# Performance work log

Hardware: AMD Instinct MI355X
Metric: run time of the kernel (lower is better)

The kernel has to match this reference:

```python
import jax, jax.numpy as jnp
import numpy as np

D_MODEL = 512
NUM_HEADS = 8
DEPTH = D_MODEL // NUM_HEADS


def setup_inputs() -> dict:
    key = jax.random.key(0)
    kx, kq, kk, kv, ko = jax.random.split(key, 5)
    scale = 1.0 / np.sqrt(D_MODEL)
    return {
        "x": jax.random.normal(kx, (4, 2048, D_MODEL), dtype=jnp.float32),
        "W_q": jax.random.normal(kq, (D_MODEL, D_MODEL), dtype=jnp.float32) * scale,
        "W_k": jax.random.normal(kk, (D_MODEL, D_MODEL), dtype=jnp.float32) * scale,
        "W_v": jax.random.normal(kv, (D_MODEL, D_MODEL), dtype=jnp.float32) * scale,
        "W_o": jax.random.normal(ko, (D_MODEL, D_MODEL), dtype=jnp.float32) * scale,
    }


def reference(x, W_q, W_k, W_v, W_o):
    B, S, _ = x.shape
    # nn.Linear with weight W: y = x @ W.T
    def split_heads(t):
        return t.reshape(B, S, NUM_HEADS, DEPTH).transpose(0, 2, 1, 3)  # [B,H,S,D]
    Q = split_heads(x @ W_q.T)
    K = split_heads(x @ W_k.T)
    V = split_heads(x @ W_v.T)
    b = -jnp.log(jnp.asarray(S, dtype=jnp.float32))  # -log(seq_len) bias
    inv_sqrt_dk = 1.0 / jnp.sqrt(jnp.asarray(DEPTH, dtype=jnp.float32))
    qk = jnp.einsum('bhqd,bhkd->bhqk', Q, K) * inv_sqrt_dk
    attn = jax.nn.sigmoid(qk + b)  # non-softmax sigmoid attention
    out = jnp.einsum('bhqk,bhkd->bhqd', attn, V)
    out = out.transpose(0, 2, 1, 3).reshape(B, S, D_MODEL)
    return out @ W_o.T
```

## Files before the change

kernel.cpp:

```cpp
#include <hip/hip_runtime.h>
#include <stdint.h>

typedef _Float16 f16x8 __attribute__((ext_vector_type(8)));
typedef _Float16 f16x4 __attribute__((ext_vector_type(4)));
typedef __fp16 h16x2 __attribute__((ext_vector_type(2)));
typedef float f32x4 __attribute__((ext_vector_type(4)));
typedef float f32x16 __attribute__((ext_vector_type(16)));

#define SEQ 2048
#define NHEADS 8

#define GLOAD_LDS16(gp, lp)                                                        \
  __builtin_amdgcn_global_load_lds(                                                \
      (const __attribute__((address_space(1))) void*)(uintptr_t)(const void*)(gp), \
      (__attribute__((address_space(3))) void*)(uintptr_t)(void*)(lp), 16, 0, 0)

#define GLD16(dst, ptr, imm) \
  asm volatile("global_load_dwordx4 %0, %1, off offset:%c2" : "=&v"(dst) : "v"(ptr), "i"(imm))

#define VMW(n)                                                     \
  do {                                                             \
    asm volatile("s_waitcnt vmcnt(%c0)" ::"i"(n) : "memory");      \
    __builtin_amdgcn_sched_barrier(0);                             \
  } while (0)

__device__ __forceinline__ f16x4 pack4(float a, float b, float c, float d) {
  h16x2 lo = __builtin_amdgcn_cvt_pkrtz(a, b);
  h16x2 hi = __builtin_amdgcn_cvt_pkrtz(c, d);
  f16x4 o;
  o.x = (_Float16)lo.x; o.y = (_Float16)lo.y;
  o.z = (_Float16)hi.x; o.w = (_Float16)hi.y;
  return o;
}

__global__ void cvt_all_kernel(const float* __restrict__ x, const float* __restrict__ wq,
                               const float* __restrict__ wk, const float* __restrict__ wv,
                               const float* __restrict__ wo, _Float16* __restrict__ xh,
                               _Float16* __restrict__ wh) {
  int i = blockIdx.x * 256 + threadIdx.x;
  const float* src;
  _Float16* dst;
  int off;
  if (i < 1048576) {
    src = x; dst = xh; off = i;
  } else {
    int j = i - 1048576;
    int sel = j >> 16;
    off = j & 65535;
    src = (sel == 0) ? wq : (sel == 1) ? wk : (sel == 2) ? wv : wo;
    dst = wh + (size_t)sel * 262144;
  }
  float4 v = ((const float4*)src)[off];
  ((f16x4*)dst)[off] = pack4(v.x, v.y, v.z, v.w);
}

__device__ __forceinline__ void gemm_tile_bt(const _Float16* __restrict__ A,
                                             const _Float16* __restrict__ B,
                                             int m0, int n0,
                                             _Float16* lds,
                                             f32x4 (&acc)[4][4]) {
  const int tid = threadIdx.x;
  const int w = tid >> 6, lane = tid & 63;
  const int wr = w >> 1, wc = w & 1;
  const int lrow = lane & 15, q = lane >> 4;
  const int snb = w * 32 + (lane >> 3);
  const int scb = lane & 7;

#pragma unroll
  for (int i = 0; i < 4; ++i)
#pragma unroll
    for (int j = 0; j < 4; ++j)
#pragma unroll
      for (int r = 0; r < 4; ++r) acc[i][j][r] = 0.f;

#pragma unroll
  for (int t = 0; t < 4; ++t) {
    int n = snb + t * 8;
    int cbg = scb ^ (n & 7);
    GLOAD_LDS16(A + (size_t)(m0 + n) * 512 + cbg * 8, lds + (w * 32 + t * 8) * 64);
    GLOAD_LDS16(B + (size_t)(n0 + n) * 512 + cbg * 8, lds + 8192 + (w * 32 + t * 8) * 64);
  }

  for (int kt = 0; kt < 8; ++kt) {
    __syncthreads();
    if (kt < 7) {
      _Float16* nb = lds + ((kt + 1) & 1) * 16384;
#pragma unroll
      for (int t = 0; t < 4; ++t) {
        int n = snb + t * 8;
        int cbg = scb ^ (n & 7);
        GLOAD_LDS16(A + (size_t)(m0 + n) * 512 + (kt + 1) * 64 + cbg * 8, nb + (w * 32 + t * 8) * 64);
        GLOAD_LDS16(B + (size_t)(n0 + n) * 512 + (kt + 1) * 64 + cbg * 8, nb + 8192 + (w * 32 + t * 8) * 64);
      }
    }
    _Float16* As = lds + (kt & 1) * 16384;
    _Float16* Bs = As + 8192;

    f16x8 af[4][2], bfr[4][2];
#pragma unroll
    for (int i = 0; i < 4; ++i) {
      int m = wr * 64 + i * 16 + lrow;
#pragma unroll
      for (int kk = 0; kk < 2; ++kk) {
        int cb = (kk * 4 + q) ^ (m & 7);
        af[i][kk] = *(const f16x8*)(As + m * 64 + cb * 8);
      }
    }
#pragma unroll
    for (int j = 0; j < 4; ++j) {
      int n = wc * 64 + j * 16 + lrow;
#pragma unroll
      for (int kk = 0; kk < 2; ++kk) {
        int cb = (kk * 4 + q) ^ (n & 7);
        bfr[j][kk] = *(const f16x8*)(Bs + n * 64 + cb * 8);
      }
    }
#pragma unroll
    for (int i = 0; i < 4; ++i)
#pragma unroll
      for (int j = 0; j < 4; ++j) {
        acc[i][j] = __builtin_amdgcn_mfma_f32_16x16x32_f16(af[i][0], bfr[j][0], acc[i][j], 0, 0, 0);
        acc[i][j] = __builtin_amdgcn_mfma_f32_16x16x32_f16(af[i][1], bfr[j][1], acc[i][j], 0, 0, 0);
      }
  }
}

__global__ __launch_bounds__(256, 2) void qkv_kernel(
    const _Float16* __restrict__ xb, const _Float16* __restrict__ Wq,
    const _Float16* __restrict__ Wk, const _Float16* __restrict__ Wv,
    _Float16* __restrict__ Qo, _Float16* __restrict__ Ko, _Float16* __restrict__ Vto) {
  __shared__ _Float16 pool[32768];
  const int z = blockIdx.z;
  f32x4 acc[4][4];
  const int tid = threadIdx.x, w = tid >> 6, lane = tid & 63;
  const int wr = w >> 1, wc = w & 1, lcol = lane & 15, q = lane >> 4;

  if (z < 2) {
    const int m0 = blockIdx.y * 128;
    const int n0 = blockIdx.x * 128;
    gemm_tile_bt((z == 0) ? Wq : Wk, xb, m0, n0, pool, acc);
    _Float16* outp = (z == 0) ? Qo : Ko;
    __syncthreads();
#pragma unroll
    for (int i = 0; i < 4; ++i) {
      int cl = wr * 64 + i * 16 + q * 4;
      int hh_l = cl >> 6, dd = cl & 63;
      int s4 = dd >> 4, hi2 = (dd >> 3) & 1, j0 = dd & 7;
#pragma unroll
      for (int j = 0; j < 4; ++j) {
        int s = wc * 64 + j * 16 + lcol;
        int blk = s >> 5, r32 = s & 31;
        int l32 = (z == 0) ? r32
                           : ((r32 & 3) | ((r32 & 4) << 1) | ((r32 & 8) >> 1) | (r32 & 16));
        *(f16x4*)(pool + (hh_l * 4 + blk) * 2048 + s4 * 512 + ((hi2 << 5) | l32) * 8 + j0) =
            pack4(acc[i][j][0], acc[i][j][1], acc[i][j][2], acc[i][j][3]);
      }
    }
    __syncthreads();
    {
      int b2 = n0 >> 11, sblk0 = (n0 & 2047) >> 5, hh0 = m0 >> 6;
#pragma unroll
      for (int rec = 0; rec < 8; ++rec) {
        int hh_l = rec >> 2, blk = rec & 3;
        size_t goff = (size_t)(b2 * NHEADS + hh0 + hh_l) * 131072 +
                      (size_t)(sblk0 + blk) * 2048;
        f16x8 vv = *(const f16x8*)(pool + rec * 2048 + tid * 8);
        *(f16x8*)(outp + goff + tid * 8) = vv;
      }
    }
  } else {
    const int m0 = blockIdx.x * 128;
    const int n0 = blockIdx.y * 128;
    gemm_tile_bt(xb, Wv, m0, n0, pool, acc);
    const int bb = m0 >> 11;
    __syncthreads();
#pragma unroll
    for (int i = 0; i < 4; ++i) {
      int s0 = wr * 64 + i * 16 + q * 4;
      int mi_l = s0 >> 5, kk = (s0 >> 4) & 1, hi2 = (s0 >> 3) & 1, j0 = s0 & 7;
#pragma unroll
      for (int j = 0; j < 4; ++j) {
        int c = wc * 64 + j * 16 + lcol;
        int hh_l = c >> 6, dd = c & 63;
        int t = dd >> 5, qq = dd & 31;
        *(f16x4*)(pool + (hh_l * 4 + mi_l) * 2048 + (kk * 2 + t) * 512 + ((hi2 << 5) | qq) * 8 + j0) =
            pack4(acc[i][j][0], acc[i][j][1], acc[i][j][2], acc[i][j][3]);
      }
    }
    __syncthreads();
    {
      int kblk0 = (m0 & 2047) >> 5, hh0 = n0 >> 6;
#pragma unroll
      for (int rec = 0; rec < 8; ++rec) {
        int hh_l = rec >> 2, mi_l = rec & 3;
        size_t goff = (size_t)(bb * NHEADS + hh0 + hh_l) * 131072 +
                      (size_t)(kblk0 + mi_l) * 2048;
        f16x8 vv = *(const f16x8*)(pool + rec * 2048 + tid * 8);
        *(f16x8*)(Vto + goff + tid * 8) = vv;
      }
    }
  }
}

__device__ __forceinline__ void attn_window(const f16x8 (&ka)[4], const f16x8 (&vb)[4],
                                            const f16x8 (&qb)[4], const f32x16& z16,
                                            f32x16& o0, f32x16& o1) {
  const float c1 = 0.18033688011112042f;
  __builtin_amdgcn_s_setprio(1);
  f32x16 s = __builtin_amdgcn_mfma_f32_32x32x16_f16(ka[0], qb[0], z16, 0, 0, 0);
  s = __builtin_amdgcn_mfma_f32_32x32x16_f16(ka[1], qb[1], s, 0, 0, 0);
  s = __builtin_amdgcn_mfma_f32_32x32x16_f16(ka[2], qb[2], s, 0, 0, 0);
  s = __builtin_amdgcn_mfma_f32_32x32x16_f16(ka[3], qb[3], s, 0, 0, 0);
  __builtin_amdgcn_s_setprio(0);

  float p[16];
#pragma unroll
  for (int r = 0; r < 16; ++r) {
    float wp = __builtin_amdgcn_exp2f(__builtin_fmaf(s[r], c1, -1.0f));
    float e = wp * 0.0009765625f;
    p[r] = __builtin_fmaf(wp, __builtin_fmaf(e, e, -e), wp);
  }

  f16x8 pa0, pa1;
  {
    h16x2 a0 = __builtin_amdgcn_cvt_pkrtz(p[0], p[1]);
    h16x2 a1 = __builtin_amdgcn_cvt_pkrtz(p[2], p[3]);
    h16x2 a2 = __builtin_amdgcn_cvt_pkrtz(p[4], p[5]);
    h16x2 a3 = __builtin_amdgcn_cvt_pkrtz(p[6], p[7]);
    pa0[0] = (_Float16)a0.x; pa0[1] = (_Float16)a0.y;
    pa0[2] = (_Float16)a1.x; pa0[3] = (_Float16)a1.y;
    pa0[4] = (_Float16)a2.x; pa0[5] = (_Float16)a2.y;
    pa0[6] = (_Float16)a3.x; pa0[7] = (_Float16)a3.y;
    h16x2 b0 = __builtin_amdgcn_cvt_pkrtz(p[8], p[9]);
    h16x2 b1 = __builtin_amdgcn_cvt_pkrtz(p[10], p[11]);
    h16x2 b2 = __builtin_amdgcn_cvt_pkrtz(p[12], p[13]);
    h16x2 b3 = __builtin_amdgcn_cvt_pkrtz(p[14], p[15]);
    pa1[0] = (_Float16)b0.x; pa1[1] = (_Float16)b0.y;
    pa1[2] = (_Float16)b1.x; pa1[3] = (_Float16)b1.y;
    pa1[4] = (_Float16)b2.x; pa1[5] = (_Float16)b2.y;
    pa1[6] = (_Float16)b3.x; pa1[7] = (_Float16)b3.y;
  }

  __builtin_amdgcn_s_setprio(1);
  o0 = __builtin_amdgcn_mfma_f32_32x32x16_f16(pa0, vb[0], o0, 0, 0, 0);
  o1 = __builtin_amdgcn_mfma_f32_32x32x16_f16(pa0, vb[1], o1, 0, 0, 0);
  o0 = __builtin_amdgcn_mfma_f32_32x32x16_f16(pa1, vb[2], o0, 0, 0, 0);
  o1 = __builtin_amdgcn_mfma_f32_32x32x16_f16(pa1, vb[3], o1, 0, 0, 0);
  __builtin_amdgcn_s_setprio(0);
}

#define ISSUE_WIN(KA, VB, KP, VP)  \
  do {                             \
    GLD16(KA[0], KP, 0);           \
    GLD16(KA[1], KP, 1024);        \
    GLD16(KA[2], KP, 2048);        \
    GLD16(KA[3], KP, 3072);        \
    GLD16(VB[0], VP, 0);           \
    GLD16(VB[1], VP, 1024);        \
    GLD16(VB[2], VP, 2048);        \
    GLD16(VB[3], VP, 3072);        \
    KP += 8192;                    \
    VP += 8192;                    \
  } while (0)

__global__ __launch_bounds__(256, 3) void attn_kernel(
    const _Float16* __restrict__ QF, const _Float16* __restrict__ KF,
    const _Float16* __restrict__ VF, _Float16* __restrict__ Ow) {
  __shared__ float Of[8704];

  const int tid = threadIdx.x, wv = tid >> 6, lane = tid & 63;
  const int q31 = lane & 31, hi = lane >> 5;

  const int L = blockIdx.x;
  const int xcd = L & 7, slot = L >> 3;
  const int bh = xcd * 4 + (slot >> 5), qt = slot & 31;
  const int b = bh >> 3, h = bh & 7;
  const int q0 = qt * 64;

  const int qi = wv & 1;
  const int kh = wv >> 1;
  const int qc = qt * 2 + qi;

  const char* qp = (const char*)QF + (size_t)bh * 262144 + qc * 4096 + lane * 16;
  const char* kpA = (const char*)KF + (size_t)bh * 262144 + (size_t)kh * 131072 + lane * 16;
  const char* kpB = kpA + 4096;
  const char* vpA = (const char*)VF + (size_t)bh * 262144 + (size_t)kh * 131072 + lane * 16;
  const char* vpB = vpA + 4096;

  f16x8 qb[4];
  GLD16(qb[0], qp, 0);
  GLD16(qb[1], qp, 1024);
  GLD16(qb[2], qp, 2048);
  GLD16(qb[3], qp, 3072);

  f16x8 kaA[4], vbA[4], kaB[4], vbB[4];
  ISSUE_WIN(kaA, vbA, kpA, vpA);
  ISSUE_WIN(kaB, vbB, kpB, vpB);

  f32x16 oacc0, oacc1, z16;
#pragma unroll
  for (int r = 0; r < 16; ++r) { z16[r] = 0.f; oacc0[r] = 0.f; oacc1[r] = 0.f; }

  for (int i = 0; i < 15; ++i) {
    VMW(8);
    attn_window(kaA, vbA, qb, z16, oacc0, oacc1);
    ISSUE_WIN(kaA, vbA, kpA, vpA);
    VMW(8);
    attn_window(kaB, vbB, qb, z16, oacc0, oacc1);
    ISSUE_WIN(kaB, vbB, kpB, vpB);
  }
  VMW(8);
  attn_window(kaA, vbA, qb, z16, oacc0, oacc1);
  VMW(0);
  attn_window(kaB, vbB, qb, z16, oacc0, oacc1);

#pragma unroll
  for (int t = 0; t < 2; ++t) {
#pragma unroll
    for (int r = 0; r < 16; ++r) {
      int row = qi * 32 + (r & 3) + ((r >> 2) << 3) + hi * 4;
      int d = t * 32 + q31;
      float v = (t == 0) ? oacc0[r] : oacc1[r];
      Of[kh * 4352 + row * 68 + d] = v * 0.0009765625f;
    }
  }
  __syncthreads();
#pragma unroll
  for (int i = 0; i < 4; ++i) {
    int o = tid * 16 + i * 4;
    int row = o >> 6, d0 = o & 63;
    f32x4 a = *(const f32x4*)(Of + row * 68 + d0);
    f32x4 c = *(const f32x4*)(Of + 4352 + row * 68 + d0);
    f16x4 v;
    v[0] = (_Float16)(a[0] + c[0]);
    v[1] = (_Float16)(a[1] + c[1]);
    v[2] = (_Float16)(a[2] + c[2]);
    v[3] = (_Float16)(a[3] + c[3]);
    *(f16x4*)(Ow + (size_t)(b * SEQ + q0 + row) * 512 + h * 64 + d0) = v;
  }
}

__global__ __launch_bounds__(256, 2) void oproj_kernel(
    const _Float16* __restrict__ A, const _Float16* __restrict__ Wo,
    float* __restrict__ out) {
  __shared__ _Float16 pool[32768];
  const int m0 = blockIdx.x * 128, n0 = blockIdx.y * 128;
  f32x4 acc[4][4];
  gemm_tile_bt(A, Wo, m0, n0, pool, acc);

  const int tid = threadIdx.x, w = tid >> 6, lane = tid & 63;
  const int wr = w >> 1, wc = w & 1, lcol = lane & 15, q = lane >> 4;
#pragma unroll
  for (int i = 0; i < 4; ++i) {
    int gm0 = m0 + wr * 64 + i * 16 + q * 4;
#pragma unroll
    for (int j = 0; j < 4; ++j) {
      int gn = n0 + wc * 64 + j * 16 + lcol;
#pragma unroll
      for (int r = 0; r < 4; ++r)
        out[(size_t)(gm0 + r) * 512 + gn] = acc[i][j][r];
    }
  }
}

extern "C" void kernel_launch(void* const* d_in, const int* in_sizes, int n_in,
                              void* d_out, int out_size, void* d_ws, size_t ws_size,
                              hipStream_t stream) {
  const float* x = (const float*)d_in[0];
  const float* Wq = (const float*)d_in[1];
  const float* Wk = (const float*)d_in[2];
  const float* Wv = (const float*)d_in[3];
  const float* Wo = (const float*)d_in[4];
  float* out = (float*)d_out;
  char* ws = (char*)d_ws;

  _Float16* xh = (_Float16*)(ws + 0);
  _Float16* wh = (_Float16*)(ws + 8388608);
  _Float16* Qw = (_Float16*)(ws + 10485760);
  _Float16* Kw = (_Float16*)(ws + 18874368);
  _Float16* Vtw = (_Float16*)(ws + 27262976);
  _Float16* Ow = (_Float16*)(ws + 35651584);

  _Float16* wqh = wh;
  _Float16* wkh = wh + 262144;
  _Float16* wvh = wh + 524288;
  _Float16* woh = wh + 786432;

  cvt_all_kernel<<<5120, 256, 0, stream>>>(x, Wq, Wk, Wv, Wo, xh, wh);
  qkv_kernel<<<dim3(64, 4, 3), 256, 0, stream>>>(xh, wqh, wkh, wvh, Qw, Kw, Vtw);
  attn_kernel<<<1024, 256, 0, stream>>>(Qw, Kw, Vtw, Ow);
  oproj_kernel<<<dim3(64, 4), 256, 0, stream>>>(Ow, woh, out);
}
```

Before: 152.6 us.

## Stage K/V windows through LDS via direct global-to-LDS loads, raise occupancy

Replaces the double-buffered register K/V prefetch with per-wave LDS staging using global_load_lds, read back with ds_read_b128 each iteration. Cutting register pressure lets launch_bounds go from 3 to 4 blocks per CU. The sigmoid polynomial is also packed into f32x2 vector FMAs. The single-buffered LDS stage forces a full vmcnt(0) wait every iteration, so load latency is only hidden by the extra occupancy rather than by in-wave prefetch.

```diff
diff --git a/kernel.cpp b/kernel.cpp
--- a/kernel.cpp
+++ b/kernel.cpp
@@ -4,6 +4,7 @@
 typedef _Float16 f16x8 __attribute__((ext_vector_type(8)));
 typedef _Float16 f16x4 __attribute__((ext_vector_type(4)));
 typedef __fp16 h16x2 __attribute__((ext_vector_type(2)));
+typedef float f32x2 __attribute__((ext_vector_type(2)));
 typedef float f32x4 __attribute__((ext_vector_type(4)));
 typedef float f32x16 __attribute__((ext_vector_type(16)));
 
@@ -18,9 +19,18 @@
 #define GLD16(dst, ptr, imm) \
   asm volatile("global_load_dwordx4 %0, %1, off offset:%c2" : "=&v"(dst) : "v"(ptr), "i"(imm))
 
+#define DSR(dst, base, imm) \
+  asm volatile("ds_read_b128 %0, %1 offset:%c2" : "=&v"(dst) : "v"(base), "i"(imm))
+
 #define VMW(n)                                                     \
   do {                                                             \
     asm volatile("s_waitcnt vmcnt(%c0)" ::"i"(n) : "memory");      \
+    __builtin_amdgcn_sched_barrier(0);                             \
+  } while (0)
+
+#define LGKM0()                                                    \
+  do {                                                             \
+    asm volatile("s_waitcnt lgkmcnt(0)" ::: "memory");             \
     __builtin_amdgcn_sched_barrier(0);                             \
   } while (0)
 
@@ -205,7 +215,6 @@
 __device__ __forceinline__ void attn_window(const f16x8 (&ka)[4], const f16x8 (&vb)[4],
                                             const f16x8 (&qb)[4], const f32x16& z16,
                                             f32x16& o0, f32x16& o1) {
-  const float c1 = 0.18033688011112042f;
   __builtin_amdgcn_s_setprio(1);
   f32x16 s = __builtin_amdgcn_mfma_f32_32x32x16_f16(ka[0], qb[0], z16, 0, 0, 0);
   s = __builtin_amdgcn_mfma_f32_32x32x16_f16(ka[1], qb[1], s, 0, 0, 0);
@@ -213,12 +222,22 @@
   s = __builtin_amdgcn_mfma_f32_32x32x16_f16(ka[3], qb[3], s, 0, 0, 0);
   __builtin_amdgcn_s_setprio(0);
 
+  const f32x2 c1v = {0.18033688011112042f, 0.18033688011112042f};
+  const f32x2 m1v = {-1.0f, -1.0f};
+  const f32x2 kv = {0.0009765625f, 0.0009765625f};
   float p[16];
 #pragma unroll
-  for (int r = 0; r < 16; ++r) {
-    float wp = __builtin_amdgcn_exp2f(__builtin_fmaf(s[r], c1, -1.0f));
-    float e = wp * 0.0009765625f;
-    p[r] = __builtin_fmaf(wp, __builtin_fmaf(e, e, -e), wp);
+  for (int r2 = 0; r2 < 8; ++r2) {
+    f32x2 s2;
+    s2.x = s[2 * r2]; s2.y = s[2 * r2 + 1];
+    f32x2 t = __builtin_elementwise_fma(s2, c1v, m1v);
+    f32x2 wp2;
+    wp2.x = __builtin_amdgcn_exp2f(t.x);
+    wp2.y = __builtin_amdgcn_exp2f(t.y);
+    f32x2 e2 = wp2 * kv;
+    f32x2 ee = __builtin_elementwise_fma(e2, e2, -e2);
+    f32x2 p2 = __builtin_elementwise_fma(wp2, ee, wp2);
+    p[2 * r2] = p2.x; p[2 * r2 + 1] = p2.y;
   }
 
   f16x8 pa0, pa1;
@@ -249,24 +268,10 @@
   __builtin_amdgcn_s_setprio(0);
 }
 
-#define ISSUE_WIN(KA, VB, KP, VP)  \
-  do {                             \
-    GLD16(KA[0], KP, 0);           \
-    GLD16(KA[1], KP, 1024);        \
-    GLD16(KA[2], KP, 2048);        \
-    GLD16(KA[3], KP, 3072);        \
-    GLD16(VB[0], VP, 0);           \
-    GLD16(VB[1], VP, 1024);        \
-    GLD16(VB[2], VP, 2048);        \
-    GLD16(VB[3], VP, 3072);        \
-    KP += 8192;                    \
-    VP += 8192;                    \
-  } while (0)
-
-__global__ __launch_bounds__(256, 3) void attn_kernel(
+__global__ __launch_bounds__(256, 4) void attn_kernel(
     const _Float16* __restrict__ QF, const _Float16* __restrict__ KF,
     const _Float16* __restrict__ VF, _Float16* __restrict__ Ow) {
-  __shared__ float Of[8704];
+  __shared__ __attribute__((aligned(16))) char smem[34816];
 
   const int tid = threadIdx.x, wv = tid >> 6, lane = tid & 63;
   const int q31 = lane & 31, hi = lane >> 5;
@@ -282,10 +287,10 @@
   const int qc = qt * 2 + qi;
 
   const char* qp = (const char*)QF + (size_t)bh * 262144 + qc * 4096 + lane * 16;
-  const char* kpA = (const char*)KF + (size_t)bh * 262144 + (size_t)kh * 131072 + lane * 16;
-  const char* kpB = kpA + 4096;
-  const char* vpA = (const char*)VF + (size_t)bh * 262144 + (size_t)kh * 131072 + lane * 16;
-  const char* vpB = vpA + 4096;
+  const char* kp = (const char*)KF + (size_t)bh * 262144 + (size_t)kh * 131072 + lane * 16;
+  const char* vp = (const char*)VF + (size_t)bh * 262144 + (size_t)kh * 131072 + lane * 16;
+
+  _Float16* stg = (_Float16*)(smem + wv * 8192);
 
   f16x8 qb[4];
   GLD16(qb[0], qp, 0);
@@ -293,27 +298,45 @@
   GLD16(qb[2], qp, 2048);
   GLD16(qb[3], qp, 3072);
 
-  f16x8 kaA[4], vbA[4], kaB[4], vbB[4];
-  ISSUE_WIN(kaA, vbA, kpA, vpA);
-  ISSUE_WIN(kaB, vbB, kpB, vpB);
+#pragma unroll
+  for (int t = 0; t < 4; ++t) GLOAD_LDS16(kp + t * 1024, stg + t * 512);
+#pragma unroll
+  for (int t = 0; t < 4; ++t) GLOAD_LDS16(vp + t * 1024, stg + 2048 + t * 512);
+  kp += 4096;
+  vp += 4096;
+  VMW(8);
 
   f32x16 oacc0, oacc1, z16;
 #pragma unroll
   for (int r = 0; r < 16; ++r) { z16[r] = 0.f; oacc0[r] = 0.f; oacc1[r] = 0.f; }
 
-  for (int i = 0; i < 15; ++i) {
-    VMW(8);
-    attn_window(kaA, vbA, qb, z16, oacc0, oacc1);
-    ISSUE_WIN(kaA, vbA, kpA, vpA);
-    VMW(8);
-    attn_window(kaB, vbB, qb, z16, oacc0, oacc1);
-    ISSUE_WIN(kaB, vbB, kpB, vpB);
-  }
-  VMW(8);
-  attn_window(kaA, vbA, qb, z16, oacc0, oacc1);
-  VMW(0);
-  attn_window(kaB, vbB, qb, z16, oacc0, oacc1);
-
+  const int dsa = wv * 8192 + lane * 16;
+
+  for (int s = 0; s < 32; ++s) {
+    VMW(0);
+    f16x8 ka[4], vb[4];
+    DSR(ka[0], dsa, 0);
+    DSR(ka[1], dsa, 1024);
+    DSR(ka[2], dsa, 2048);
+    DSR(ka[3], dsa, 3072);
+    DSR(vb[0], dsa, 4096);
+    DSR(vb[1], dsa, 5120);
+    DSR(vb[2], dsa, 6144);
+    DSR(vb[3], dsa, 7168);
+    LGKM0();
+    if (s < 31) {
+#pragma unroll
+      for (int t = 0; t < 4; ++t) GLOAD_LDS16(kp + t * 1024, stg + t * 512);
+#pragma unroll
+      for (int t = 0; t < 4; ++t) GLOAD_LDS16(vp + t * 1024, stg + 2048 + t * 512);
+      kp += 4096;
+      vp += 4096;
+    }
+    attn_window(ka, vb, qb, z16, oacc0, oacc1);
+  }
+
+  __syncthreads();
+  float* Of = (float*)smem;
 #pragma unroll
   for (int t = 0; t < 2; ++t) {
 #pragma unroll
```

New measurement: 158.0 us. 3.6% more time.
